# Performance work log

Hardware: AMD Instinct MI355X
Metric: run time of the kernel (lower is better)

## Reference

```python
import jax, jax.numpy as jnp
import numpy as np

N = 50000      # nodes
E = 800000     # edges (before self loops)
D = 128        # node feat dim (in = hidden = out)
R_IN = 64      # edge feat in
R_OUT = 64     # edge feat out


def setup_inputs() -> dict:
    key = jax.random.key(0)
    ks = jax.random.split(key, 10)
    src = jax.random.randint(ks[0], (E,), 0, N, dtype=jnp.int32)
    dst = jax.random.randint(ks[1], (E,), 0, N, dtype=jnp.int32)
    x = jax.random.normal(ks[2], (N, D), jnp.float32)
    text_h = jax.random.normal(ks[3], (E, R_IN), jnp.float32)
    s = 1.0 / np.sqrt(D)
    W1 = jax.random.normal(ks[4], (D, D), jnp.float32) * s
    b1 = jnp.zeros((D,), jnp.float32)
    W2 = jax.random.normal(ks[5], (D, D), jnp.float32) * s
    b2 = jnp.zeros((D,), jnp.float32)
    sr = 1.0 / np.sqrt(R_IN)
    relW = jax.random.normal(ks[6], (R_IN, R_OUT), jnp.float32) * sr
    relb = jnp.zeros((R_OUT,), jnp.float32)
    return {"src": src, "dst": dst, "x": x, "text_h": text_h,
            "W1": W1, "b1": b1, "W2": W2, "b2": b2,
            "relW": relW, "relb": relb}


def _graph_conv(h, src, dst, norm_src, norm_dst, W, b, n):
    # DGL GraphConv, norm='both': scale src, gather, segment-sum to dst, scale dst, linear, relu
    h = h * norm_src                                   # [N, D]
    agg = jax.ops.segment_sum(h[src], dst, num_segments=n)  # [N, D]
    h = agg * norm_dst
    return jax.nn.relu(h @ W + b)


def reference(src, dst, x, text_h, W1, b1, W2, b2, relW, relb):
    n = x.shape[0]
    loop = jnp.arange(n, dtype=src.dtype)
    src_a = jnp.concatenate([src, loop])               # add_self_loop
    dst_a = jnp.concatenate([dst, loop])
    ones = jnp.ones(src_a.shape[0], x.dtype)
    out_deg = jax.ops.segment_sum(ones, src_a, num_segments=n)
    in_deg = jax.ops.segment_sum(ones, dst_a, num_segments=n)
    norm_src = (out_deg ** -0.5)[:, None]              # >=1 thanks to self loops
    norm_dst = (in_deg ** -0.5)[:, None]
    h = _graph_conv(x, src_a, dst_a, norm_src, norm_dst, W1, b1, n)
    h = _graph_conv(h, src_a, dst_a, norm_src, norm_dst, W2, b2, n)
    # apply_edges: rel_linear on text_h (self-loop edges get zero-filled text_h)
    text_all = jnp.concatenate([text_h, jnp.zeros((n, text_h.shape[1]), text_h.dtype)])
    e_h = text_all @ relW + relb                       # [E+N, R_OUT]
    # apply_nodes: activation applied once more
    h = jax.nn.relu(h)
    return h, e_h
```

## Files before the change

kernel.cpp:

```cpp
#include <hip/hip_runtime.h>

constexpr int D = 128;
constexpr int R = 64;
constexpr int CAP = 64;
constexpr int OVF_CAP = 65536;
constexpr int TPAD = 68;

typedef float floatx4 __attribute__((ext_vector_type(4)));

static __device__ __forceinline__ float4 f4fma(float a, float4 w, float4 c) {
  c.x = fmaf(a, w.x, c.x); c.y = fmaf(a, w.y, c.y);
  c.z = fmaf(a, w.z, c.z); c.w = fmaf(a, w.w, c.w);
  return c;
}

static __device__ __forceinline__ void nt_store4(float4 v, float* p) {
  floatx4 q; q.x = v.x; q.y = v.y; q.z = v.z; q.w = v.w;
  __builtin_nontemporal_store(q, (floatx4*)p);
}

static __device__ __forceinline__ float selk(float4 a, int kk) {
  return (kk == 0) ? a.x : (kk == 1) ? a.y : (kk == 2) ? a.z : a.w;
}

static __device__ __forceinline__ unsigned pack_bf16x2(float lo, float hi) {
  unsigned ulo = __float_as_uint(lo), uhi = __float_as_uint(hi);
  ulo += 0x7FFFu + ((ulo >> 16) & 1u);
  uhi += 0x7FFFu + ((uhi >> 16) & 1u);
  return (ulo >> 16) | (uhi & 0xFFFF0000u);
}
static __device__ __forceinline__ float bf_lo(unsigned u) { return __uint_as_float(u << 16); }
static __device__ __forceinline__ float bf_hi(unsigned u) { return __uint_as_float(u & 0xFFFF0000u); }

__global__ void k_init(int* deg_out, int* cursor, int* ovf_cnt, int n) {
  int i = blockIdx.x * blockDim.x + threadIdx.x;
  if (i < n) { deg_out[i] = 1; cursor[i] = 0; }
  if (i == 0) ovf_cnt[0] = 0;
}

__global__ void k_fill(const int* __restrict__ src, const int* __restrict__ dst,
                       int* deg_out, int* cursor, int* bucket,
                       int* ovf_cnt, int2* ovf, int e) {
  int i = blockIdx.x * blockDim.x + threadIdx.x;
  if (i >= e) return;
  int d = dst[i], s = src[i];
  atomicAdd(&deg_out[s], 1);
  int slot = atomicAdd(&cursor[d], 1);
  if (slot < CAP) bucket[(size_t)d * CAP + slot] = s;
  else {
    int oi = atomicAdd(ovf_cnt, 1);
    if (oi < OVF_CAP) ovf[oi] = make_int2(s, d);
  }
}

__global__ void k_norm(const int* __restrict__ deg_out, const int* __restrict__ cursor,
                       float* ns, float* nd, int n) {
  int i = blockIdx.x * blockDim.x + threadIdx.x;
  if (i < n) {
    ns[i] = rsqrtf((float)deg_out[i]);
    nd[i] = rsqrtf((float)(cursor[i] + 1));
  }
}

__global__ __launch_bounds__(256) void k_prep(const float* __restrict__ X,
                                              const float* __restrict__ ns,
                                              uint4* __restrict__ xs, int n16) {
  int idx = blockIdx.x * 256 + threadIdx.x;
  if (idx >= n16) return;
  int row = idx >> 4, g = idx & 15;
  const float4* xp = (const float4*)(X + (size_t)row * D + g * 8);
  float4 a = xp[0], b = xp[1];
  float s = ns[row];
  uint4 o;
  o.x = pack_bf16x2(a.x * s, a.y * s);
  o.y = pack_bf16x2(a.z * s, a.w * s);
  o.z = pack_bf16x2(b.x * s, b.y * s);
  o.w = pack_bf16x2(b.z * s, b.w * s);
  xs[(size_t)row * 16 + g] = o;
}

__global__ __launch_bounds__(256) void k_agg_b(const unsigned* __restrict__ XS,
                                               const int* __restrict__ cursor,
                                               const int* __restrict__ bucket,
                                               float* __restrict__ agg, int n) {
  int g = threadIdx.x >> 5, lane = threadIdx.x & 31;
  int v = blockIdx.x * 8 + g;
  if (v >= n) return;
  float4 acc;
  {
    uint2 u = ((const uint2*)(XS + (size_t)v * 64))[lane];
    acc.x = bf_lo(u.x); acc.y = bf_hi(u.x); acc.z = bf_lo(u.y); acc.w = bf_hi(u.y);
  }
  int cnt = min(cursor[v], CAP);
  const int* bk = bucket + (size_t)v * CAP;
  int i = 0;
  for (; i + 4 <= cnt; i += 4) {
    int s0 = bk[i], s1 = bk[i + 1], s2 = bk[i + 2], s3 = bk[i + 3];
    uint2 u0 = ((const uint2*)(XS + (size_t)s0 * 64))[lane];
    uint2 u1 = ((const uint2*)(XS + (size_t)s1 * 64))[lane];
    uint2 u2 = ((const uint2*)(XS + (size_t)s2 * 64))[lane];
    uint2 u3 = ((const uint2*)(XS + (size_t)s3 * 64))[lane];
    acc.x += bf_lo(u0.x) + bf_lo(u1.x) + bf_lo(u2.x) + bf_lo(u3.x);
    acc.y += bf_hi(u0.x) + bf_hi(u1.x) + bf_hi(u2.x) + bf_hi(u3.x);
    acc.z += bf_lo(u0.y) + bf_lo(u1.y) + bf_lo(u2.y) + bf_lo(u3.y);
    acc.w += bf_hi(u0.y) + bf_hi(u1.y) + bf_hi(u2.y) + bf_hi(u3.y);
  }
  for (; i < cnt; ++i) {
    int s0 = bk[i];
    uint2 u0 = ((const uint2*)(XS + (size_t)s0 * 64))[lane];
    acc.x += bf_lo(u0.x); acc.y += bf_hi(u0.x);
    acc.z += bf_lo(u0.y); acc.w += bf_hi(u0.y);
  }
  ((float4*)(agg + (size_t)v * D))[lane] = acc;
}

__global__ __launch_bounds__(128) void k_ovf_b(const unsigned* __restrict__ XS,
                                               const int* __restrict__ ovf_cnt,
                                               const int2* __restrict__ ovf,
                                               float* agg) {
  int m = min(ovf_cnt[0], OVF_CAP);
  int t = threadIdx.x;
  for (int i = blockIdx.x; i < m; i += gridDim.x) {
    int2 e = ovf[i];
    unsigned u = XS[(size_t)e.x * 64 + (t >> 1)];
    float f = (t & 1) ? bf_hi(u) : bf_lo(u);
    atomicAdd(&agg[(size_t)e.y * D + t], f);
  }
}

__global__ __launch_bounds__(256) void k_gemm_relu(const float* __restrict__ A,
                                                   const float* __restrict__ ndv,
                                                   const float* __restrict__ W,
                                                   const float* __restrict__ bias,
                                                   const float* __restrict__ post,
                                                   float* __restrict__ outf,
                                                   unsigned* __restrict__ outb,
                                                   int n) {
  __shared__ float Wl[D * D];
  int t = threadIdx.x;
  for (int i = t; i < (D * D) / 4; i += 256) ((float4*)Wl)[i] = ((const float4*)W)[i];
  __syncthreads();

  int ct = t & 15, rg = t >> 4;
  int c0 = ct << 2;
  int row0 = blockIdx.x * 64;

  float4 bb0 = *(const float4*)(bias + c0);
  float4 bb1 = *(const float4*)(bias + c0 + 64);

  int r[4]; const float4* Ap[4];
#pragma unroll
  for (int m = 0; m < 4; ++m) {
    r[m] = row0 + rg + 16 * m;
    int rc = (r[m] < n) ? r[m] : (n - 1);
    Ap[m] = (const float4*)(A + (size_t)rc * D);
  }

  float4 acc[4][2];
#pragma unroll
  for (int m = 0; m < 4; ++m) {
    acc[m][0] = make_float4(0.f, 0.f, 0.f, 0.f);
    acc[m][1] = make_float4(0.f, 0.f, 0.f, 0.f);
  }

#pragma unroll 8
  for (int k4 = 0; k4 < 32; ++k4) {
    float4 a0 = Ap[0][k4], a1 = Ap[1][k4], a2 = Ap[2][k4], a3 = Ap[3][k4];
    const float* wbase = Wl + (k4 << 9) + c0;
#pragma unroll
    for (int kk = 0; kk < 4; ++kk) {
      float4 w0 = *(const float4*)(wbase + (kk << 7));
      float4 w1 = *(const float4*)(wbase + (kk << 7) + 64);
      float e0 = selk(a0, kk), e1 = selk(a1, kk), e2 = selk(a2, kk), e3 = selk(a3, kk);
      acc[0][0] = f4fma(e0, w0, acc[0][0]); acc[0][1] = f4fma(e0, w1, acc[0][1]);
      acc[1][0] = f4fma(e1, w0, acc[1][0]); acc[1][1] = f4fma(e1, w1, acc[1][1]);
      acc[2][0] = f4fma(e2, w0, acc[2][0]); acc[2][1] = f4fma(e2, w1, acc[2][1]);
      acc[3][0] = f4fma(e3, w0, acc[3][0]); acc[3][1] = f4fma(e3, w1, acc[3][1]);
    }
  }

#pragma unroll
  for (int m = 0; m < 4; ++m) {
    if (r[m] < n) {
      float ndr = ndv[r[m]];
      float4 o0, o1;
      o0.x = fmaxf(fmaf(acc[m][0].x, ndr, bb0.x), 0.f);
      o0.y = fmaxf(fmaf(acc[m][0].y, ndr, bb0.y), 0.f);
      o0.z = fmaxf(fmaf(acc[m][0].z, ndr, bb0.z), 0.f);
      o0.w = fmaxf(fmaf(acc[m][0].w, ndr, bb0.w), 0.f);
      o1.x = fmaxf(fmaf(acc[m][1].x, ndr, bb1.x), 0.f);
      o1.y = fmaxf(fmaf(acc[m][1].y, ndr, bb1.y), 0.f);
      o1.z = fmaxf(fmaf(acc[m][1].z, ndr, bb1.z), 0.f);
      o1.w = fmaxf(fmaf(acc[m][1].w, ndr, bb1.w), 0.f);
      if (outb) {
        float ps = post[r[m]];
        uint2 p0, p1;
        p0.x = pack_bf16x2(o0.x * ps, o0.y * ps);
        p0.y = pack_bf16x2(o0.z * ps, o0.w * ps);
        p1.x = pack_bf16x2(o1.x * ps, o1.y * ps);
        p1.y = pack_bf16x2(o1.z * ps, o1.w * ps);
        *(uint2*)(outb + (size_t)r[m] * 64 + (c0 >> 1)) = p0;
        *(uint2*)(outb + (size_t)r[m] * 64 + (c0 >> 1) + 32) = p1;
      } else {
        *(float4*)(outf + (size_t)r[m] * D + c0) = o0;
        *(float4*)(outf + (size_t)r[m] * D + c0 + 64) = o1;
      }
    }
  }
}

__global__ __launch_bounds__(256) void k_rel(const float* __restrict__ T,
                                             const float* __restrict__ Wr,
                                             const float* __restrict__ br,
                                             float* __restrict__ out,
                                             int e, int ntot) {
  __shared__ float Wl[R * R];
  __shared__ float Tl[64 * TPAD];
  int t = threadIdx.x;
  int tile = blockIdx.x;
  const float4 z4 = make_float4(0.f, 0.f, 0.f, 0.f);

  float4 pre[4];
#pragma unroll
  for (int j = 0; j < 4; ++j) {
    int q = t + 256 * j, rr = q >> 4, c4 = q & 15;
    int grow = tile * 64 + rr;
    pre[j] = (grow < e) ? ((const float4*)T)[(size_t)grow * 16 + c4] : z4;
  }
  for (int i = t; i < (R * R) / 4; i += 256) ((float4*)Wl)[i] = ((const float4*)Wr)[i];
#pragma unroll
  for (int j = 0; j < 4; ++j) {
    int q = t + 256 * j, rr = q >> 4, c4 = q & 15;
    *(float4*)&Tl[rr * TPAD + (c4 << 2)] = pre[j];
  }
  __syncthreads();

  int ct = t & 15, rg = t >> 4;
  int c0 = ct << 2;
  float4 bb = *(const float4*)(br + c0);

  float4 acc0 = bb, acc1 = bb, acc2 = bb, acc3 = bb;
#pragma unroll 4
  for (int k4 = 0; k4 < 16; ++k4) {
    float4 a0 = *(const float4*)&Tl[(rg     ) * TPAD + (k4 << 2)];
    float4 a1 = *(const float4*)&Tl[(rg + 16) * TPAD + (k4 << 2)];
    float4 a2 = *(const float4*)&Tl[(rg + 32) * TPAD + (k4 << 2)];
    float4 a3 = *(const float4*)&Tl[(rg + 48) * TPAD + (k4 << 2)];
    const float* wbase = Wl + (k4 << 8) + c0;
#pragma unroll
    for (int kk = 0; kk < 4; ++kk) {
      float4 w = *(const float4*)(wbase + (kk << 6));
      float e0 = selk(a0, kk), e1 = selk(a1, kk), e2 = selk(a2, kk), e3 = selk(a3, kk);
      acc0 = f4fma(e0, w, acc0);
      acc1 = f4fma(e1, w, acc1);
      acc2 = f4fma(e2, w, acc2);
      acc3 = f4fma(e3, w, acc3);
    }
  }

  int base = tile * 64;
  if (base + rg      < ntot) nt_store4(acc0, out + (size_t)(base + rg     ) * R + c0);
  if (base + rg + 16 < ntot) nt_store4(acc1, out + (size_t)(base + rg + 16) * R + c0);
  if (base + rg + 32 < ntot) nt_store4(acc2, out + (size_t)(base + rg + 32) * R + c0);
  if (base + rg + 48 < ntot) nt_store4(acc3, out + (size_t)(base + rg + 48) * R + c0);
}

extern "C" void kernel_launch(void* const* d_in, const int* in_sizes, int n_in,
                              void* d_out, int out_size, void* d_ws, size_t ws_size,
                              hipStream_t stream) {
  const int*   src  = (const int*)d_in[0];
  const int*   dst  = (const int*)d_in[1];
  const float* x    = (const float*)d_in[2];
  const float* text = (const float*)d_in[3];
  const float* W1   = (const float*)d_in[4];
  const float* b1   = (const float*)d_in[5];
  const float* W2   = (const float*)d_in[6];
  const float* b2   = (const float*)d_in[7];
  const float* relW = (const float*)d_in[8];
  const float* relb = (const float*)d_in[9];

  const int E = in_sizes[0];
  const int N = in_sizes[2] / D;

  float* outH = (float*)d_out;
  float* outE = outH + (size_t)N * D;

  char* w = (char*)d_ws;
  auto alloc = [&](size_t bytes) -> void* {
    void* p = (void*)w;
    w += (bytes + 255) & ~(size_t)255;
    return p;
  };
  int*      deg_out  = (int*)alloc((size_t)N * 4);
  int*      cursor   = (int*)alloc((size_t)N * 4);
  float*    norm_src = (float*)alloc((size_t)N * 4);
  float*    norm_dst = (float*)alloc((size_t)N * 4);
  int*      ovf_cnt  = (int*)alloc(256);
  int2*     ovf      = (int2*)alloc((size_t)OVF_CAP * 8);
  int*      bucket   = (int*)alloc((size_t)N * CAP * 4);
  float*    agg      = (float*)alloc((size_t)N * D * 4);
  unsigned* xs       = (unsigned*)alloc((size_t)N * 64 * 4);
  unsigned* h1p      = (unsigned*)alloc((size_t)N * 64 * 4);

  int nbN = (N + 255) / 256;
  int nbE = (E + 255) / 256;

  k_init<<<nbN, 256, 0, stream>>>(deg_out, cursor, ovf_cnt, N);
  k_fill<<<nbE, 256, 0, stream>>>(src, dst, deg_out, cursor, bucket, ovf_cnt, ovf, E);
  k_norm<<<nbN, 256, 0, stream>>>(deg_out, cursor, norm_src, norm_dst, N);

  k_prep<<<(N * 16 + 255) / 256, 256, 0, stream>>>(x, norm_src, (uint4*)xs, N * 16);
  k_agg_b<<<(N + 7) / 8, 256, 0, stream>>>(xs, cursor, bucket, agg, N);
  k_ovf_b<<<64, 128, 0, stream>>>(xs, ovf_cnt, ovf, agg);
  k_gemm_relu<<<(N + 63) / 64, 256, 0, stream>>>(agg, norm_dst, W1, b1, norm_src,
                                                 nullptr, h1p, N);

  k_agg_b<<<(N + 7) / 8, 256, 0, stream>>>(h1p, cursor, bucket, agg, N);
  k_ovf_b<<<64, 128, 0, stream>>>(h1p, ovf_cnt, ovf, agg);
  k_gemm_relu<<<(N + 63) / 64, 256, 0, stream>>>(agg, norm_dst, W2, b2, nullptr,
                                                 outH, nullptr, N);

  int ntot = E + N;
  int nTiles = (ntot + 63) / 64;
  k_rel<<<nTiles, 256, 0, stream>>>(text, relW, relb, outE, E, ntot);
}
```

Measured before the change: 372.4 us.

## Compute edge relation linear with bf16 MFMA instead of fp32 FMA

Replaces the LDS-tiled fp32 FMA kernel for the edge relation linear with a kernel that uses MFMA 16x16x32 bf16 instructions. Weight fragments are loaded directly into registers per wave, and text rows are read straight from global memory and converted to bf16 with no shared memory staging. The aim is to cut compute and LDS overhead so this stage runs at memory bandwidth. The cost is bf16 rounding of both the inputs and the weights, and output stores become scalar per-lane writes rather than float4.

```diff
diff --git a/kernel.cpp b/kernel.cpp
--- a/kernel.cpp
+++ b/kernel.cpp
@@ -4,9 +4,10 @@
 constexpr int R = 64;
 constexpr int CAP = 64;
 constexpr int OVF_CAP = 65536;
-constexpr int TPAD = 68;
 
 typedef float floatx4 __attribute__((ext_vector_type(4)));
+typedef short bf16x8 __attribute__((ext_vector_type(8)));
+typedef float f32x4 __attribute__((ext_vector_type(4)));
 
 static __device__ __forceinline__ float4 f4fma(float a, float4 w, float4 c) {
   c.x = fmaf(a, w.x, c.x); c.y = fmaf(a, w.y, c.y);
@@ -28,6 +29,11 @@
   ulo += 0x7FFFu + ((ulo >> 16) & 1u);
   uhi += 0x7FFFu + ((uhi >> 16) & 1u);
   return (ulo >> 16) | (uhi & 0xFFFF0000u);
+}
+static __device__ __forceinline__ short f2bf(float f) {
+  unsigned u = __float_as_uint(f);
+  u += 0x7FFFu + ((u >> 16) & 1u);
+  return (short)(u >> 16);
 }
 static __device__ __forceinline__ float bf_lo(unsigned u) { return __uint_as_float(u << 16); }
 static __device__ __forceinline__ float bf_hi(unsigned u) { return __uint_as_float(u & 0xFFFF0000u); }
@@ -209,60 +215,65 @@
   }
 }
 
-__global__ __launch_bounds__(256) void k_rel(const float* __restrict__ T,
-                                             const float* __restrict__ Wr,
-                                             const float* __restrict__ br,
-                                             float* __restrict__ out,
-                                             int e, int ntot) {
-  __shared__ float Wl[R * R];
-  __shared__ float Tl[64 * TPAD];
-  int t = threadIdx.x;
-  int tile = blockIdx.x;
+__global__ __launch_bounds__(256) void k_rel_mfma(const float* __restrict__ T,
+                                                  const float* __restrict__ Wr,
+                                                  const float* __restrict__ br,
+                                                  float* __restrict__ out,
+                                                  int e, int ntot) {
+  int l = threadIdx.x & 63;
+  int wid = threadIdx.x >> 6;
+  int lr = l & 15;
+  int kg = l >> 4;
+
+  bf16x8 bfrag[4][2];
+#pragma unroll
+  for (int ct = 0; ct < 4; ++ct)
+#pragma unroll
+    for (int h = 0; h < 2; ++h) {
+      const float* wp = Wr + (size_t)(h * 32 + kg * 8) * 64 + ct * 16 + lr;
+#pragma unroll
+      for (int i = 0; i < 8; ++i) bfrag[ct][h][i] = f2bf(wp[(size_t)i * 64]);
+    }
+
+  float bias[4];
+#pragma unroll
+  for (int ct = 0; ct < 4; ++ct) bias[ct] = br[ct * 16 + lr];
+
+  int base = blockIdx.x * 128 + wid * 32;
   const float4 z4 = make_float4(0.f, 0.f, 0.f, 0.f);
 
-  float4 pre[4];
-#pragma unroll
-  for (int j = 0; j < 4; ++j) {
-    int q = t + 256 * j, rr = q >> 4, c4 = q & 15;
-    int grow = tile * 64 + rr;
-    pre[j] = (grow < e) ? ((const float4*)T)[(size_t)grow * 16 + c4] : z4;
-  }
-  for (int i = t; i < (R * R) / 4; i += 256) ((float4*)Wl)[i] = ((const float4*)Wr)[i];
-#pragma unroll
-  for (int j = 0; j < 4; ++j) {
-    int q = t + 256 * j, rr = q >> 4, c4 = q & 15;
-    *(float4*)&Tl[rr * TPAD + (c4 << 2)] = pre[j];
-  }
-  __syncthreads();
-
-  int ct = t & 15, rg = t >> 4;
-  int c0 = ct << 2;
-  float4 bb = *(const float4*)(br + c0);
-
-  float4 acc0 = bb, acc1 = bb, acc2 = bb, acc3 = bb;
-#pragma unroll 4
-  for (int k4 = 0; k4 < 16; ++k4) {
-    float4 a0 = *(const float4*)&Tl[(rg     ) * TPAD + (k4 << 2)];
-    float4 a1 = *(const float4*)&Tl[(rg + 16) * TPAD + (k4 << 2)];
-    float4 a2 = *(const float4*)&Tl[(rg + 32) * TPAD + (k4 << 2)];
-    float4 a3 = *(const float4*)&Tl[(rg + 48) * TPAD + (k4 << 2)];
-    const float* wbase = Wl + (k4 << 8) + c0;
-#pragma unroll
-    for (int kk = 0; kk < 4; ++kk) {
-      float4 w = *(const float4*)(wbase + (kk << 6));
-      float e0 = selk(a0, kk), e1 = selk(a1, kk), e2 = selk(a2, kk), e3 = selk(a3, kk);
-      acc0 = f4fma(e0, w, acc0);
-      acc1 = f4fma(e1, w, acc1);
-      acc2 = f4fma(e2, w, acc2);
-      acc3 = f4fma(e3, w, acc3);
-    }
-  }
-
-  int base = tile * 64;
-  if (base + rg      < ntot) nt_store4(acc0, out + (size_t)(base + rg     ) * R + c0);
-  if (base + rg + 16 < ntot) nt_store4(acc1, out + (size_t)(base + rg + 16) * R + c0);
-  if (base + rg + 32 < ntot) nt_store4(acc2, out + (size_t)(base + rg + 32) * R + c0);
-  if (base + rg + 48 < ntot) nt_store4(acc3, out + (size_t)(base + rg + 48) * R + c0);
+#pragma unroll
+  for (int g = 0; g < 2; ++g) {
+    int R0 = base + g * 16;
+    int row = R0 + lr;
+    bool v = row < e;
+    const float4* tp = (const float4*)(T + (size_t)(v ? row : 0) * 64);
+
+    bf16x8 afrag[2];
+#pragma unroll
+    for (int h = 0; h < 2; ++h) {
+      float4 a0 = v ? tp[kg * 2 + h * 8]     : z4;
+      float4 a1 = v ? tp[kg * 2 + h * 8 + 1] : z4;
+      afrag[h][0] = f2bf(a0.x); afrag[h][1] = f2bf(a0.y);
+      afrag[h][2] = f2bf(a0.z); afrag[h][3] = f2bf(a0.w);
+      afrag[h][4] = f2bf(a1.x); afrag[h][5] = f2bf(a1.y);
+      afrag[h][6] = f2bf(a1.z); afrag[h][7] = f2bf(a1.w);
+    }
+
+#pragma unroll
+    for (int ct = 0; ct < 4; ++ct) {
+      f32x4 acc;
+      acc[0] = bias[ct]; acc[1] = bias[ct]; acc[2] = bias[ct]; acc[3] = bias[ct];
+      acc = __builtin_amdgcn_mfma_f32_16x16x32_bf16(afrag[0], bfrag[ct][0], acc, 0, 0, 0);
+      acc = __builtin_amdgcn_mfma_f32_16x16x32_bf16(afrag[1], bfrag[ct][1], acc, 0, 0, 0);
+#pragma unroll
+      for (int r = 0; r < 4; ++r) {
+        int orow = R0 + kg * 4 + r;
+        if (orow < ntot)
+          __builtin_nontemporal_store(acc[r], out + (size_t)orow * R + ct * 16 + lr);
+      }
+    }
+  }
 }
 
 extern "C" void kernel_launch(void* const* d_in, const int* in_sizes, int n_in,
@@ -321,6 +332,6 @@
                                                  outH, nullptr, N);
 
   int ntot = E + N;
-  int nTiles = (ntot + 63) / 64;
-  k_rel<<<nTiles, 256, 0, stream>>>(text, relW, relb, outE, E, ntot);
-}
+  int nBlk = (ntot + 127) / 128;
+  k_rel_mfma<<<nBlk, 256, 0, stream>>>(text, relW, relb, outE, E, ntot);
+}
```

Measured after the change: 388.2 us. +4.2%, slower.
